# Performance work log

Measured on AMD Instinct MI355X. Metric: run time of the kernel, lower is better.

## Reference

```python
import jax, jax.numpy as jnp
import numpy as np

N = 30000        # nodes
E = 480000       # edges (before self-loops)
F_IN = 512       # input feature dim
HID = 64         # per-head hidden dim
HEADS = 4
WIDTH = HID * HEADS  # 256, concat heads
LAYERS = 3
NCLS = 40
NEG_SLOPE = 0.2


def setup_inputs() -> dict:
    key = jax.random.key(0)
    ks = jax.random.split(key, 16)
    def p(k, shape, scale=0.1):
        return jax.random.normal(k, shape, dtype=jnp.float32) * scale
    return {
        "x": jax.random.normal(ks[0], (N, F_IN), dtype=jnp.float32),
        "edge_index": jax.random.randint(ks[1], (2, E), 0, N, dtype=jnp.int32),
        # layer 1: F_IN -> HEADS*HID (concat)
        "W1": p(ks[2], (F_IN, WIDTH)), "as1": p(ks[3], (HEADS, HID)), "ad1": p(ks[4], (HEADS, HID)), "b1": p(ks[5], (WIDTH,)),
        # layer 2: WIDTH -> WIDTH
        "W2": p(ks[6], (WIDTH, WIDTH)), "as2": p(ks[7], (HEADS, HID)), "ad2": p(ks[8], (HEADS, HID)), "b2": p(ks[9], (WIDTH,)),
        # layer 3: WIDTH -> WIDTH
        "W3": p(ks[10], (WIDTH, WIDTH)), "as3": p(ks[11], (HEADS, HID)), "ad3": p(ks[12], (HEADS, HID)), "b3": p(ks[13], (WIDTH,)),
        # JK='cat' output head: WIDTH*LAYERS -> NCLS
        "Wo": p(ks[14], (WIDTH * LAYERS, NCLS)), "bo": p(ks[15], (NCLS,)),
    }


def gat_layer(x, Wm, a_src, a_dst, b, src, dst):
    # PyG GATConv (concat=True, eval mode): h = xW reshaped [N,H,C];
    # e_ij = leaky_relu(a_src.h_j + a_dst.h_i) for edge j->i, softmax over dst groups.
    n = x.shape[0]
    H, C = a_src.shape
    h = (x @ Wm).reshape(n, H, C)                      # [N,H,C]
    es = jnp.sum(h * a_src, axis=-1)                   # [N,H]
    ed = jnp.sum(h * a_dst, axis=-1)                   # [N,H]
    e = jax.nn.leaky_relu(es[src] + ed[dst], NEG_SLOPE)  # [Etot,H]
    m = jax.ops.segment_max(e, dst, num_segments=n)    # stable softmax per dst node
    w = jnp.exp(e - m[dst])
    den = jax.ops.segment_sum(w, dst, num_segments=n)
    alpha = w / den[dst]                               # [Etot,H]
    out = jax.ops.segment_sum(h[src] * alpha[:, :, None], dst, num_segments=n)  # [N,H,C]
    return out.reshape(n, H * C) + b


def reference(x, edge_index, W1, as1, ad1, b1, W2, as2, ad2, b2, W3, as3, ad3, b3, Wo, bo):
    # add self-loops (PyG GATConv default)
    loops = jnp.arange(N, dtype=edge_index.dtype)
    src = jnp.concatenate([edge_index[0], loops])
    dst = jnp.concatenate([edge_index[1], loops])
    # dropout is identity in eval mode
    h1 = jax.nn.relu(gat_layer(x, W1, as1, ad1, b1, src, dst))
    h2 = jax.nn.relu(gat_layer(h1, W2, as2, ad2, b2, src, dst))
    h3 = jax.nn.relu(gat_layer(h2, W3, as3, ad3, b3, src, dst))
    h = jnp.concatenate([h1, h2, h3], axis=-1)         # JK 'cat': [N, WIDTH*LAYERS]
    return h @ Wo + bo                                 # [N, NCLS]
```

## Files before the change

kernel.cpp:

```cpp
#include <hip/hip_runtime.h>

#define N_NODES 30000
#define N_EDGES 480000
#define ETOT    510000
#define F_IN    512
#define WIDTH   256
#define NCLS    40
#define KCAT    768
#define NPAD    48
#define TM      64
#define BROWS   272

typedef __attribute__((ext_vector_type(8))) short short8;
typedef __attribute__((ext_vector_type(4))) float f32x4;

__device__ __forceinline__ unsigned short f2bf(float f){
  unsigned u = __float_as_uint(f);
  u += 0x7fffu + ((u >> 16) & 1u);
  return (unsigned short)(u >> 16);
}
__device__ __forceinline__ float b2f(unsigned short s){
  return __uint_as_float(((unsigned)s) << 16);
}

__device__ __forceinline__ void gload_lds16(const void* g, void* l){
  __builtin_amdgcn_global_load_lds(
      (const __attribute__((address_space(1))) unsigned int*)g,
      (__attribute__((address_space(3))) unsigned int*)l, 16, 0, 0);
}

__device__ __forceinline__ void av_body(const float* __restrict__ W,
                                        const float* __restrict__ a_s,
                                        const float* __restrict__ a_d,
                                        unsigned short* __restrict__ Bt, int K, int k){
  int tid = threadIdx.x;
  int h = tid >> 6, lane = tid & 63;
  float wv = W[(size_t)k * WIDTH + tid];
  float ps = wv * a_s[tid];
  float pd = wv * a_d[tid];
  #pragma unroll
  for (int off = 32; off; off >>= 1){
    ps += __shfl_down(ps, off, 64);
    pd += __shfl_down(pd, off, 64);
  }
  if (lane == 0){
    Bt[(size_t)(256 + h) * K + k] = f2bf(ps);
    Bt[(size_t)(260 + h) * K + k] = f2bf(pd);
  }
  if (tid < 8) Bt[(size_t)(264 + tid) * K + k] = 0;
}

#define PREP_GRID (118 + 512 + 256 + 256 + 144 + 512 + 256 + 256)

__global__ __launch_bounds__(256) void prep_kernel(
    const float* __restrict__ W1, const float* __restrict__ as1, const float* __restrict__ ad1,
    const float* __restrict__ W2, const float* __restrict__ as2, const float* __restrict__ ad2,
    const float* __restrict__ W3, const float* __restrict__ as3, const float* __restrict__ ad3,
    const float* __restrict__ Wo,
    unsigned short* __restrict__ Wt1, unsigned short* __restrict__ Wt2,
    unsigned short* __restrict__ Wt3, unsigned short* __restrict__ WoT,
    int* __restrict__ counts){
  int b = blockIdx.x, tid = threadIdx.x;
  if (b < 118){
    int i = b * 256 + tid;
    if (i < N_NODES) counts[i] = 0;
    return;
  }
  b -= 118;
  if (b < 512){
    int n = b >> 1, k = (b & 1) * 256 + tid;
    Wt1[(size_t)n * F_IN + k] = f2bf(W1[(size_t)k * WIDTH + n]);
    return;
  }
  b -= 512;
  if (b < 256){ Wt2[(size_t)b * WIDTH + tid] = f2bf(W2[(size_t)tid * WIDTH + b]); return; }
  b -= 256;
  if (b < 256){ Wt3[(size_t)b * WIDTH + tid] = f2bf(W3[(size_t)tid * WIDTH + b]); return; }
  b -= 256;
  if (b < 144){
    int i = b * 256 + tid;
    int c = i / KCAT, k = i - c * KCAT;
    WoT[i] = (c < NCLS) ? f2bf(Wo[(size_t)k * NCLS + c]) : (unsigned short)0;
    return;
  }
  b -= 144;
  if (b < 512){ av_body(W1, as1, ad1, Wt1, F_IN, b); return; }
  b -= 512;
  if (b < 256){ av_body(W2, as2, ad2, Wt2, WIDTH, b); return; }
  b -= 256;
  av_body(W3, as3, ad3, Wt3, WIDTH, b);
}

__global__ void hist_kernel(const int* __restrict__ ei, int* __restrict__ counts){
  int e = blockIdx.x * blockDim.x + threadIdx.x;
  if (e < ETOT){
    int d = (e < N_EDGES) ? ei[N_EDGES + e] : (e - N_EDGES);
    atomicAdd(&counts[d], 1);
  }
}

__global__ __launch_bounds__(1024) void scan_part_kernel(const int* __restrict__ counts,
                                                         int* __restrict__ offsets,
                                                         int* __restrict__ bsum, int n){
  __shared__ int wsum[16];
  int tid = threadIdx.x, lane = tid & 63, wid = tid >> 6;
  int i = blockIdx.x * 1024 + tid;
  int v = (i < n) ? counts[i] : 0;
  int x = v;
  #pragma unroll
  for (int off = 1; off < 64; off <<= 1){
    int t = __shfl_up(x, off, 64);
    if (lane >= off) x += t;
  }
  if (lane == 63) wsum[wid] = x;
  __syncthreads();
  if (wid == 0){
    int s = (lane < 16) ? wsum[lane] : 0;
    #pragma unroll
    for (int off = 1; off < 16; off <<= 1){
      int t = __shfl_up(s, off, 64);
      if (lane >= off) s += t;
    }
    if (lane < 16) wsum[lane] = s;
  }
  __syncthreads();
  int wp = (wid > 0) ? wsum[wid - 1] : 0;
  if (i < n) offsets[i] = x - v + wp;
  if (tid == 0) bsum[blockIdx.x] = wsum[15];
}

__global__ __launch_bounds__(64) void scan_bsum_kernel(int* __restrict__ bsum,
                                                       int* __restrict__ offsets,
                                                       int nb, int n){
  int lane = threadIdx.x;
  int v = (lane < nb) ? bsum[lane] : 0;
  int x = v;
  #pragma unroll
  for (int off = 1; off < 64; off <<= 1){
    int t = __shfl_up(x, off, 64);
    if (lane >= off) x += t;
  }
  if (lane < nb) bsum[lane] = x - v;
  if (lane == nb - 1) offsets[n] = x;
}

__global__ __launch_bounds__(1024) void scan_add_kernel(int* __restrict__ offsets,
                                                        int* __restrict__ cursor,
                                                        const int* __restrict__ bsum, int n){
  int i = blockIdx.x * 1024 + threadIdx.x;
  if (i < n){
    int o = offsets[i] + bsum[blockIdx.x];
    offsets[i] = o;
    cursor[i] = o;
  }
}

template<int K, bool AF32>
__global__ __launch_bounds__(512, 4)
void gemm_bres_kernel(const void* __restrict__ Araw,
                      const unsigned short* __restrict__ Bt,
                      float* __restrict__ es,
                      float* __restrict__ ed,
                      unsigned short* __restrict__ hb,
                      int M, int ngb,
                      const int* __restrict__ ei,
                      int* __restrict__ cursor,
                      int* __restrict__ srcs){
  constexpr int KT = K / 32;
  constexpr int NP = K / 256;
  constexpr int KE = KT / 8;
  __shared__ unsigned short Abuf[TM * 256];
  __shared__ float cmbE[8][TM][9];

  int tid = threadIdx.x;

  if ((int)blockIdx.x >= ngb){
    int e = ((int)blockIdx.x - ngb) * 512 + tid;
    if (e < ETOT){
      int s, d;
      if (e < N_EDGES){ s = ei[e]; d = ei[N_EDGES + e]; }
      else { s = e - N_EDGES; d = s; }
      int pos = atomicAdd(&cursor[d], 1);
      srcs[pos] = s;
    }
    return;
  }

  int lane = tid & 63, w = tid >> 6;
  int l15 = lane & 15, quad = lane >> 4;
  int c0 = w * 32;
  int r0 = blockIdx.x * TM;

  f32x4 acc[4][2];
  #pragma unroll
  for (int s = 0; s < 4; ++s){
    acc[s][0] = (f32x4){0.f,0.f,0.f,0.f};
    acc[s][1] = (f32x4){0.f,0.f,0.f,0.f};
  }

  #pragma unroll 1
  for (int p = 0; p < NP; ++p){
    if (p) __syncthreads();
    if constexpr (AF32){
      const char* xb = (const char*)Araw;
      uint4 va[8];
      #pragma unroll
      for (int i = 0; i < 8; ++i){
        int L32 = (i * 512 + tid) * 16;
        int row = L32 >> 10;
        int colb = L32 & 1023;
        int grow = r0 + row; if (grow > M - 1) grow = M - 1;
        va[i] = *(const uint4*)(xb + (size_t)grow * (K*4) + p*1024 + colb);
      }
      #pragma unroll
      for (int i = 0; i < 8; ++i){
        int ob = (i * 512 + tid) * 8;
        int row = ob >> 9;
        unsigned u0 = (unsigned)f2bf(__uint_as_float(va[i].x)) |
                      ((unsigned)f2bf(__uint_as_float(va[i].y)) << 16);
        unsigned u1 = (unsigned)f2bf(__uint_as_float(va[i].z)) |
                      ((unsigned)f2bf(__uint_as_float(va[i].w)) << 16);
        uint2 uv; uv.x = u0; uv.y = u1;
        *(uint2*)((char*)Abuf + (ob ^ ((row & 7) << 4))) = uv;
      }
    } else {
      const char* Ab = (const char*)Araw;
      #pragma unroll
      for (int c = 0; c < 4; ++c){
        int L = (c * 512 + tid) * 16;
        int row = L >> 9;
        int colb = L & 511;
        int grow = r0 + row; if (grow > M - 1) grow = M - 1;
        gload_lds16(Ab + (size_t)grow * (K*2) + p*512 + (colb ^ ((row & 7) << 4)),
                    (char*)Abuf + L);
      }
    }
    __syncthreads();

    #pragma unroll 1
    for (int sb = 0; sb < 2; ++sb){
      short8 Bf[4][2];
      #pragma unroll
      for (int kt2 = 0; kt2 < 4; ++kt2){
        #pragma unroll
        for (int ct = 0; ct < 2; ++ct){
          Bf[kt2][ct] = *(const short8*)(Bt + (size_t)(c0 + ct*16 + l15) * K
                                            + (p*8 + sb*4 + kt2)*32 + quad*8);
        }
      }
      __builtin_amdgcn_sched_barrier(0);
      #pragma unroll
      for (int s = 0; s < 4; ++s){
        int row = s * 16 + l15;
        int swzus = (row & 7) << 3;
        const unsigned short* base = Abuf + row * 256;
        #pragma unroll
        for (int kt2 = 0; kt2 < 4; ++kt2){
          short8 af = *(const short8*)(base + (((sb*4 + kt2)*32 + quad*8) ^ swzus));
          acc[s][0] = __builtin_amdgcn_mfma_f32_16x16x32_bf16(af, Bf[kt2][0], acc[s][0], 0, 0, 0);
          acc[s][1] = __builtin_amdgcn_mfma_f32_16x16x32_bf16(af, Bf[kt2][1], acc[s][1], 0, 0, 0);
        }
      }
    }

    if (w * KE >= p * 8 && w * KE < p * 8 + 8){
      short8 Bfe[KE];
      #pragma unroll
      for (int i = 0; i < KE; ++i){
        Bfe[i] = *(const short8*)(Bt + (size_t)(256 + l15) * K + (w*KE + i)*32 + quad*8);
      }
      f32x4 eacc[4];
      #pragma unroll
      for (int s = 0; s < 4; ++s) eacc[s] = (f32x4){0.f,0.f,0.f,0.f};
      #pragma unroll
      for (int s = 0; s < 4; ++s){
        int row = s * 16 + l15;
        int swzus = (row & 7) << 3;
        const unsigned short* base = Abuf + row * 256;
        #pragma unroll
        for (int i = 0; i < KE; ++i){
          int kt2 = w*KE + i - p*8;
          short8 af = *(const short8*)(base + ((kt2*32 + quad*8) ^ swzus));
          eacc[s] = __builtin_amdgcn_mfma_f32_16x16x32_bf16(af, Bfe[i], eacc[s], 0, 0, 0);
        }
      }
      #pragma unroll
      for (int s = 0; s < 4; ++s){
        #pragma unroll
        for (int r = 0; r < 4; ++r){
          int row = s * 16 + quad * 4 + r;
          if (l15 < 8) cmbE[w][row][l15] = eacc[s][r];
        }
      }
    }
  }

  __syncthreads();
  #pragma unroll
  for (int s = 0; s < 4; ++s){
    #pragma unroll
    for (int r = 0; r < 4; ++r){
      int row = s * 16 + quad * 4 + r;
      int swz = (row & 7) << 4;
      #pragma unroll
      for (int ct = 0; ct < 2; ++ct){
        int colb = (c0 + ct * 16 + l15) * 2;
        *(unsigned short*)((char*)Abuf + ((row * 512 + colb) ^ swz))
            = f2bf(acc[s][ct][r]);
      }
    }
  }
  __syncthreads();

  #pragma unroll
  for (int c = 0; c < 4; ++c){
    int us = (c * 512 + tid) * 8;
    int row = us >> 8, col = us & 255;
    int grow = r0 + row;
    if (grow < M){
      uint4 v = *(const uint4*)((const char*)Abuf + ((row * 512 + col * 2) ^ ((row & 7) << 4)));
      *(uint4*)(hb + (size_t)grow * WIDTH + col) = v;
    }
  }
  {
    int row = tid >> 3, j = tid & 7;
    int grow = r0 + row;
    if (grow < M){
      float v = 0.f;
      #pragma unroll
      for (int ww = 0; ww < 8; ++ww) v += cmbE[ww][row][j];
      if (j < 4) es[(size_t)grow * 4 + j] = v;
      else       ed[(size_t)grow * 4 + (j - 4)] = v;
    }
  }
}

__global__ __launch_bounds__(256) void agg_kernel(const int* __restrict__ offsets,
                                                  const int* __restrict__ srcs,
                                                  const float* __restrict__ es,
                                                  const float* __restrict__ ed,
                                                  const unsigned short* __restrict__ hb,
                                                  const float* __restrict__ bias,
                                                  unsigned short* __restrict__ hout){
  __shared__ float eLds[8][64][4];
  __shared__ int   sLds[8][64];
  int wid = threadIdx.x >> 6;
  int lane = threadIdx.x & 63;
  int half = lane >> 5, l32 = lane & 31;
  int slot = wid * 2 + half;
  int n = blockIdx.x * 8 + slot;
  int base = offsets[n];
  int deg = offsets[n + 1] - base;
  float4 edv = *(const float4*)(ed + (size_t)n * 4);

  float m0 = -1e30f, m1 = -1e30f, m2 = -1e30f, m3 = -1e30f;
  for (int i = l32; i < deg; i += 32){
    int s = srcs[base + i];
    float4 ev = *(const float4*)(es + (size_t)s * 4);
    float e0 = ev.x + edv.x, e1 = ev.y + edv.y, e2 = ev.z + edv.z, e3 = ev.w + edv.w;
    e0 = e0 > 0.f ? e0 : 0.2f * e0;
    e1 = e1 > 0.f ? e1 : 0.2f * e1;
    e2 = e2 > 0.f ? e2 : 0.2f * e2;
    e3 = e3 > 0.f ? e3 : 0.2f * e3;
    if (i < 64){
      sLds[slot][i] = s;
      *(float4*)(&eLds[slot][i][0]) = (float4){e0, e1, e2, e3};
    }
    m0 = fmaxf(m0, e0); m1 = fmaxf(m1, e1); m2 = fmaxf(m2, e2); m3 = fmaxf(m3, e3);
  }
  #pragma unroll
  for (int off = 1; off < 32; off <<= 1){
    m0 = fmaxf(m0, __shfl_xor(m0, off, 64));
    m1 = fmaxf(m1, __shfl_xor(m1, off, 64));
    m2 = fmaxf(m2, __shfl_xor(m2, off, 64));
    m3 = fmaxf(m3, __shfl_xor(m3, off, 64));
  }
  int head = l32 >> 3;
  float mh  = (head == 0) ? m0 : (head == 1) ? m1 : (head == 2) ? m2 : m3;
  float edh = (head == 0) ? edv.x : (head == 1) ? edv.y : (head == 2) ? edv.z : edv.w;

  float2 a0 = {0.f,0.f}, a1 = {0.f,0.f}, a2 = {0.f,0.f}, a3 = {0.f,0.f};
  float den = 0.f;
  const unsigned short* hcol = hb + 8 * l32;
  for (int i = 0; i < deg; i += 8){
    int sidx[8]; float wgt[8];
    #pragma unroll
    for (int u = 0; u < 8; ++u){
      int idx = i + u;
      bool v = idx < deg;
      float le; int s;
      if (idx < 64 || !v){
        int ic = v ? idx : 0;
        if (ic >= 64) ic = 0;
        s  = sLds[slot][ic];
        le = eLds[slot][ic][head];
      } else {
        s = srcs[base + idx];
        float e = es[(size_t)s * 4 + head] + edh;
        le = e > 0.f ? e : 0.2f * e;
      }
      sidx[u] = s;
      wgt[u] = v ? __expf(le - mh) : 0.f;
    }
    uint4 hv[8];
    #pragma unroll
    for (int u = 0; u < 8; ++u)
      hv[u] = *(const uint4*)(hcol + (size_t)sidx[u] * WIDTH);
    #pragma unroll
    for (int u = 0; u < 8; ++u){
      float wu = wgt[u];
      den += wu;
      a0.x += wu * __uint_as_float(hv[u].x << 16);
      a0.y += wu * __uint_as_float(hv[u].x & 0xffff0000u);
      a1.x += wu * __uint_as_float(hv[u].y << 16);
      a1.y += wu * __uint_as_float(hv[u].y & 0xffff0000u);
      a2.x += wu * __uint_as_float(hv[u].z << 16);
      a2.y += wu * __uint_as_float(hv[u].z & 0xffff0000u);
      a3.x += wu * __uint_as_float(hv[u].w << 16);
      a3.y += wu * __uint_as_float(hv[u].w & 0xffff0000u);
    }
  }
  float inv = 1.0f / den;
  const float* bp = bias + 8 * l32;
  float4 bv0 = *(const float4*)(bp);
  float4 bv1 = *(const float4*)(bp + 4);
  float o0 = fmaxf(a0.x * inv + bv0.x, 0.f);
  float o1 = fmaxf(a0.y * inv + bv0.y, 0.f);
  float o2 = fmaxf(a1.x * inv + bv0.z, 0.f);
  float o3 = fmaxf(a1.y * inv + bv0.w, 0.f);
  float o4 = fmaxf(a2.x * inv + bv1.x, 0.f);
  float o5 = fmaxf(a2.y * inv + bv1.y, 0.f);
  float o6 = fmaxf(a3.x * inv + bv1.z, 0.f);
  float o7 = fmaxf(a3.y * inv + bv1.w, 0.f);
  uint4 o;
  o.x = (unsigned)f2bf(o0) | ((unsigned)f2bf(o1) << 16);
  o.y = (unsigned)f2bf(o2) | ((unsigned)f2bf(o3) << 16);
  o.z = (unsigned)f2bf(o4) | ((unsigned)f2bf(o5) << 16);
  o.w = (unsigned)f2bf(o6) | ((unsigned)f2bf(o7) << 16);
  *(uint4*)(hout + (size_t)n * WIDTH + 8 * l32) = o;
}

__global__ __launch_bounds__(256) void out_gemm_kernel(const unsigned short* __restrict__ h1,
                                                       const unsigned short* __restrict__ h2,
                                                       const unsigned short* __restrict__ h3,
                                                       const unsigned short* __restrict__ WoT,
                                                       const float* __restrict__ bo,
                                                       float* __restrict__ out){
  int tid = threadIdx.x, lane = tid & 63, wid = tid >> 6;
  int l15 = lane & 15, quad = lane >> 4;
  int m0 = blockIdx.x * 64 + 16 * wid;

  f32x4 acc[3];
  #pragma unroll
  for (int t = 0; t < 3; ++t) acc[t] = (f32x4){0.f, 0.f, 0.f, 0.f};

  int arow = m0 + l15; if (arow >= N_NODES) arow = N_NODES - 1;

  #pragma unroll
  for (int part = 0; part < 3; ++part){
    const unsigned short* hp = (part == 0) ? h1 : (part == 1) ? h2 : h3;
    const unsigned short* ap = hp + (size_t)arow * WIDTH;
    #pragma unroll
    for (int k0 = 0; k0 < WIDTH; k0 += 32){
      short8 af = *(const short8*)(ap + k0 + quad * 8);
      int kk = part * WIDTH + k0;
      #pragma unroll
      for (int t = 0; t < 3; ++t){
        short8 bf = *(const short8*)(WoT + (size_t)(16 * t + l15) * KCAT + kk + quad * 8);
        acc[t] = __builtin_amdgcn_mfma_f32_16x16x32_bf16(af, bf, acc[t], 0, 0, 0);
      }
    }
  }

  int r0 = m0 + quad * 4;
  #pragma unroll
  for (int t = 0; t < 3; ++t){
    int col = 16 * t + l15;
    if (col < NCLS){
      float bc = bo[col];
      #pragma unroll
      for (int r = 0; r < 4; ++r){
        int grow = r0 + r;
        if (grow < N_NODES) out[(size_t)grow * NCLS + col] = acc[t][r] + bc;
      }
    }
  }
}

static inline size_t align256(size_t x){ return (x + 255) & ~(size_t)255; }

extern "C" void kernel_launch(void* const* d_in, const int* in_sizes, int n_in,
                              void* d_out, int out_size, void* d_ws, size_t ws_size,
                              hipStream_t stream) {
  const float* x   = (const float*)d_in[0];
  const int*   ei  = (const int*)  d_in[1];
  const float* W1  = (const float*)d_in[2];
  const float* as1 = (const float*)d_in[3];
  const float* ad1 = (const float*)d_in[4];
  const float* b1  = (const float*)d_in[5];
  const float* W2  = (const float*)d_in[6];
  const float* as2 = (const float*)d_in[7];
  const float* ad2 = (const float*)d_in[8];
  const float* b2  = (const float*)d_in[9];
  const float* W3  = (const float*)d_in[10];
  const float* as3 = (const float*)d_in[11];
  const float* ad3 = (const float*)d_in[12];
  const float* b3  = (const float*)d_in[13];
  const float* Wo  = (const float*)d_in[14];
  const float* bo  = (const float*)d_in[15];
  float* out = (float*)d_out;

  char* p = (char*)d_ws;
  auto take = [&](size_t bytes) -> char* { char* cur = p; p += align256(bytes); return cur; };

  unsigned short* Wt1   = (unsigned short*)take((size_t)BROWS * F_IN * 2);
  unsigned short* Wt2   = (unsigned short*)take((size_t)BROWS * WIDTH * 2);
  unsigned short* Wt3   = (unsigned short*)take((size_t)BROWS * WIDTH * 2);
  unsigned short* WoT   = (unsigned short*)take((size_t)NPAD * KCAT * 2);
  unsigned short* hs    = (unsigned short*)take((size_t)N_NODES * WIDTH * 2);
  float*          es    = (float*)take((size_t)N_NODES * 4 * 4);
  float*          ed    = (float*)take((size_t)N_NODES * 4 * 4);
  unsigned short* h1b   = (unsigned short*)take((size_t)N_NODES * WIDTH * 2);
  unsigned short* h2b   = (unsigned short*)take((size_t)N_NODES * WIDTH * 2);
  unsigned short* h3b   = (unsigned short*)take((size_t)N_NODES * WIDTH * 2);
  int*            counts  = (int*)take((size_t)N_NODES * 4);
  int*            offsets = (int*)take((size_t)(N_NODES + 1) * 4);
  int*            cursor  = (int*)take((size_t)N_NODES * 4);
  int*            srcs    = (int*)take((size_t)ETOT * 4);
  int*            bsum    = (int*)take((size_t)64 * 4);

  prep_kernel<<<PREP_GRID, 256, 0, stream>>>(W1, as1, ad1, W2, as2, ad2,
                                             W3, as3, ad3, Wo,
                                             Wt1, Wt2, Wt3, WoT, counts);

  const int nb = (N_NODES + 1023) / 1024;
  hist_kernel<<<(ETOT + 255) / 256, 256, 0, stream>>>(ei, counts);
  scan_part_kernel<<<nb, 1024, 0, stream>>>(counts, offsets, bsum, N_NODES);
  scan_bsum_kernel<<<1, 64, 0, stream>>>(bsum, offsets, nb, N_NODES);
  scan_add_kernel<<<nb, 1024, 0, stream>>>(offsets, cursor, bsum, N_NODES);

  const int ntiles = (N_NODES + TM - 1) / TM;
  const int nscat  = (ETOT + 511) / 512;
  const int agg_grid = N_NODES / 8;
  const int out_grid = (N_NODES + 63) / 64;

  gemm_bres_kernel<F_IN, true><<<ntiles + nscat, 512, 0, stream>>>(
      x, Wt1, es, ed, hs, N_NODES, ntiles, ei, cursor, srcs);
  agg_kernel<<<agg_grid, 256, 0, stream>>>(offsets, srcs, es, ed, hs, b1, h1b);
  gemm_bres_kernel<WIDTH, false><<<ntiles, 512, 0, stream>>>(
      h1b, Wt2, es, ed, hs, N_NODES, ntiles, ei, cursor, srcs);
  agg_kernel<<<agg_grid, 256, 0, stream>>>(offsets, srcs, es, ed, hs, b2, h2b);
  gemm_bres_kernel<WIDTH, false><<<ntiles, 512, 0, stream>>>(
      h2b, Wt3, es, ed, hs, N_NODES, ntiles, ei, cursor, srcs);
  agg_kernel<<<agg_grid, 256, 0, stream>>>(offsets, srcs, es, ed, hs, b3, h3b);

  out_gemm_kernel<<<out_grid, 256, 0, stream>>>(h1b, h2b, h3b, WoT, bo, out);
}
```

Baseline: 361.6 us.

## Fuse histogram into prep kernel and use single-pass decoupled lookback scan

Moves the degree histogram into the prep kernel, with counts zeroed by a memset, and replaces the three-kernel scan with one kernel that uses decoupled lookback over per-block state flags. This removes three kernel launches and the dependent round trips between them. The lookback depends on predecessor blocks being resident or already finished, which holds for only 30 blocks but adds spin-waiting.

```diff
diff --git a/kernel.cpp b/kernel.cpp
--- a/kernel.cpp
+++ b/kernel.cpp
@@ -50,23 +50,33 @@
   if (tid < 8) Bt[(size_t)(264 + tid) * K + k] = 0;
 }
 
-#define PREP_GRID (118 + 512 + 256 + 256 + 144 + 512 + 256 + 256)
+#define NHIST 1993
+#define PREP_GRID (NHIST + 1 + 512 + 256 + 256 + 144 + 512 + 256 + 256)
 
 __global__ __launch_bounds__(256) void prep_kernel(
+    const int* __restrict__ ei, int* __restrict__ counts,
+    unsigned long long* __restrict__ bstate,
     const float* __restrict__ W1, const float* __restrict__ as1, const float* __restrict__ ad1,
     const float* __restrict__ W2, const float* __restrict__ as2, const float* __restrict__ ad2,
     const float* __restrict__ W3, const float* __restrict__ as3, const float* __restrict__ ad3,
     const float* __restrict__ Wo,
     unsigned short* __restrict__ Wt1, unsigned short* __restrict__ Wt2,
-    unsigned short* __restrict__ Wt3, unsigned short* __restrict__ WoT,
-    int* __restrict__ counts){
+    unsigned short* __restrict__ Wt3, unsigned short* __restrict__ WoT){
   int b = blockIdx.x, tid = threadIdx.x;
-  if (b < 118){
-    int i = b * 256 + tid;
-    if (i < N_NODES) counts[i] = 0;
+  if (b < NHIST){
+    int e = b * 256 + tid;
+    if (e < ETOT){
+      int d = (e < N_EDGES) ? ei[N_EDGES + e] : (e - N_EDGES);
+      atomicAdd(&counts[d], 1);
+    }
     return;
   }
-  b -= 118;
+  b -= NHIST;
+  if (b < 1){
+    if (tid < 64) bstate[tid] = 0ull;
+    return;
+  }
+  b -= 1;
   if (b < 512){
     int n = b >> 1, k = (b & 1) * 256 + tid;
     Wt1[(size_t)n * F_IN + k] = f2bf(W1[(size_t)k * WIDTH + n]);
@@ -91,20 +101,16 @@
   av_body(W3, as3, ad3, Wt3, WIDTH, b);
 }
 
-__global__ void hist_kernel(const int* __restrict__ ei, int* __restrict__ counts){
-  int e = blockIdx.x * blockDim.x + threadIdx.x;
-  if (e < ETOT){
-    int d = (e < N_EDGES) ? ei[N_EDGES + e] : (e - N_EDGES);
-    atomicAdd(&counts[d], 1);
-  }
-}
-
-__global__ __launch_bounds__(1024) void scan_part_kernel(const int* __restrict__ counts,
-                                                         int* __restrict__ offsets,
-                                                         int* __restrict__ bsum, int n){
+__global__ __launch_bounds__(1024) void scan_kernel(const int* __restrict__ counts,
+                                                    int* __restrict__ offsets,
+                                                    int* __restrict__ cursor,
+                                                    unsigned long long* __restrict__ bstate,
+                                                    int n, int nb){
   __shared__ int wsum[16];
+  __shared__ int sbase;
   int tid = threadIdx.x, lane = tid & 63, wid = tid >> 6;
-  int i = blockIdx.x * 1024 + tid;
+  int b = blockIdx.x;
+  int i = b * 1024 + tid;
   int v = (i < n) ? counts[i] : 0;
   int x = v;
   #pragma unroll
@@ -125,31 +131,30 @@
   }
   __syncthreads();
   int wp = (wid > 0) ? wsum[wid - 1] : 0;
-  if (i < n) offsets[i] = x - v + wp;
-  if (tid == 0) bsum[blockIdx.x] = wsum[15];
-}
-
-__global__ __launch_bounds__(64) void scan_bsum_kernel(int* __restrict__ bsum,
-                                                       int* __restrict__ offsets,
-                                                       int nb, int n){
-  int lane = threadIdx.x;
-  int v = (lane < nb) ? bsum[lane] : 0;
-  int x = v;
-  #pragma unroll
-  for (int off = 1; off < 64; off <<= 1){
-    int t = __shfl_up(x, off, 64);
-    if (lane >= off) x += t;
-  }
-  if (lane < nb) bsum[lane] = x - v;
-  if (lane == nb - 1) offsets[n] = x;
-}
-
-__global__ __launch_bounds__(1024) void scan_add_kernel(int* __restrict__ offsets,
-                                                        int* __restrict__ cursor,
-                                                        const int* __restrict__ bsum, int n){
-  int i = blockIdx.x * 1024 + threadIdx.x;
+  int bsum = wsum[15];
+  if (tid == 0){
+    unsigned long long pk = ((unsigned long long)(unsigned)bsum << 32) | (b == 0 ? 2ull : 1ull);
+    __hip_atomic_store(&bstate[b], pk, __ATOMIC_RELEASE, __HIP_MEMORY_SCOPE_AGENT);
+    int excl = 0;
+    for (int j = b - 1; j >= 0; ){
+      unsigned long long st = __hip_atomic_load(&bstate[j], __ATOMIC_ACQUIRE, __HIP_MEMORY_SCOPE_AGENT);
+      unsigned fl = (unsigned)(st & 3u);
+      if (fl == 0u) continue;
+      excl += (int)(st >> 32);
+      if (fl == 2u) break;
+      --j;
+    }
+    if (b > 0){
+      unsigned long long pk2 = ((unsigned long long)(unsigned)(excl + bsum) << 32) | 2ull;
+      __hip_atomic_store(&bstate[b], pk2, __ATOMIC_RELEASE, __HIP_MEMORY_SCOPE_AGENT);
+    }
+    if (b == nb - 1) offsets[n] = excl + bsum;
+    sbase = excl;
+  }
+  __syncthreads();
+  int base = sbase;
   if (i < n){
-    int o = offsets[i] + bsum[blockIdx.x];
+    int o = x - v + wp + base;
     offsets[i] = o;
     cursor[i] = o;
   }
@@ -527,17 +532,17 @@
   int*            offsets = (int*)take((size_t)(N_NODES + 1) * 4);
   int*            cursor  = (int*)take((size_t)N_NODES * 4);
   int*            srcs    = (int*)take((size_t)ETOT * 4);
-  int*            bsum    = (int*)take((size_t)64 * 4);
-
-  prep_kernel<<<PREP_GRID, 256, 0, stream>>>(W1, as1, ad1, W2, as2, ad2,
+  unsigned long long* bstate = (unsigned long long*)take((size_t)64 * 8);
+
+  hipMemsetAsync(counts, 0, (size_t)N_NODES * 4, stream);
+
+  prep_kernel<<<PREP_GRID, 256, 0, stream>>>(ei, counts, bstate,
+                                             W1, as1, ad1, W2, as2, ad2,
                                              W3, as3, ad3, Wo,
-                                             Wt1, Wt2, Wt3, WoT, counts);
+                                             Wt1, Wt2, Wt3, WoT);
 
   const int nb = (N_NODES + 1023) / 1024;
-  hist_kernel<<<(ETOT + 255) / 256, 256, 0, stream>>>(ei, counts);
-  scan_part_kernel<<<nb, 1024, 0, stream>>>(counts, offsets, bsum, N_NODES);
-  scan_bsum_kernel<<<1, 64, 0, stream>>>(bsum, offsets, nb, N_NODES);
-  scan_add_kernel<<<nb, 1024, 0, stream>>>(offsets, cursor, bsum, N_NODES);
+  scan_kernel<<<nb, 1024, 0, stream>>>(counts, offsets, cursor, bstate, N_NODES, nb);
 
   const int ntiles = (N_NODES + TM - 1) / TM;
   const int nscat  = (ETOT + 511) / 512;
```

Result: no change. 365.4 us (+1.1%).
